# Kernel tuning notes

Measured on AMD Instinct MI355X. Metric: run time of the kernel, lower is better.

## Reference

```python
import jax, jax.numpy as jnp
import numpy as np

HEADS = 16
HEAD_DIM = 128
ROPE_BASE = 10000.0

def _rope_tables(T, D):
    # inv_freq over even indices, freqs = outer(pos, inv_freq), emb = concat([freqs, freqs])
    inv_freq = 1.0 / (ROPE_BASE ** (jnp.arange(0, D, 2, dtype=jnp.float32) / D))
    t = jnp.arange(T, dtype=jnp.float32)
    freqs = t[:, None] * inv_freq[None, :]          # (T, D/2)
    emb = jnp.concatenate([freqs, freqs], axis=-1)  # (T, D)
    return jnp.cos(emb), jnp.sin(emb)

def _rotate_half(x):
    half = x.shape[-1] // 2
    x1, x2 = x[..., :half], x[..., half:]
    return jnp.concatenate([-x2, x1], axis=-1)

def setup_inputs() -> dict:
    key = jax.random.key(0)
    k1, k2, k3 = jax.random.split(key, 3)
    B, T, dim = 2, 2048, 2048
    inner = HEADS * HEAD_DIM
    x = jax.random.normal(k1, (B, T, dim), dtype=jnp.float32)
    W_qkv = jax.random.normal(k2, (3 * inner, dim), dtype=jnp.float32) * 0.02
    W_proj = jax.random.normal(k3, (dim, inner), dtype=jnp.float32) * 0.02
    return {"x": x, "W_qkv": W_qkv, "W_proj": W_proj}

def reference(x, W_qkv, W_proj):
    B, T, dim = x.shape
    H, D = HEADS, HEAD_DIM
    # QKV projection (Linear with weight (out, in): y = x @ W^T)
    qkv = jnp.einsum('btd,ed->bte', x, W_qkv)          # (B, T, 3*H*D)
    q, k, v = jnp.split(qkv, 3, axis=-1)
    def to_heads(t):
        return t.reshape(B, T, H, D).transpose(0, 2, 1, 3)  # (B, H, T, D)
    q, k, v = to_heads(q), to_heads(k), to_heads(v)
    # RoPE, offset = 0 (uncached path)
    cos, sin = _rope_tables(T, D)                      # (T, D)
    cos = cos[None, None]
    sin = sin[None, None]
    q = q * cos + _rotate_half(q) * sin
    k = k * cos + _rotate_half(k) * sin
    # causal SDPA
    scale = 1.0 / jnp.sqrt(jnp.float32(D))
    scores = jnp.einsum('bhqd,bhkd->bhqk', q, k) * scale
    causal = jnp.tril(jnp.ones((T, T), dtype=bool))
    scores = jnp.where(causal[None, None], scores, jnp.finfo(scores.dtype).min)
    attn = jax.nn.softmax(scores, axis=-1)
    out = jnp.einsum('bhqk,bhkd->bhqd', attn, v)       # (B, H, T, D)
    out = out.transpose(0, 2, 1, 3).reshape(B, T, H * D)
    return jnp.einsum('bti,oi->bto', out, W_proj)      # (B, T, dim)
```

## Files before the change

kernel.cpp:

```cpp
#include <hip/hip_runtime.h>
#include <hip/hip_bf16.h>
#include <stdint.h>

typedef __attribute__((ext_vector_type(8))) short short8;
typedef __attribute__((ext_vector_type(4))) float f32x4;

#define HEADS 16
#define HDIM  128
#define BB    2
#define TT    2048
#define DMODEL 2048
#define INNER 2048
#define E3    6144
#define NTOK  (BB*TT)

__device__ inline void store1(__hip_bfloat16* p, float v) { *p = __float2bfloat16(v); }
__device__ inline void store1(float* p, float v)          { *p = v; }

__device__ inline short bfbits(float v) {
  __hip_bfloat16 h = __float2bfloat16(v);
  return *(short*)&h;
}

__device__ inline void gl_lds16(const __hip_bfloat16* g, __hip_bfloat16* l) {
  __builtin_amdgcn_global_load_lds(
      (const __attribute__((address_space(1))) void*)g,
      (__attribute__((address_space(3))) void*)l, 16, 0, 0);
}

__global__ __launch_bounds__(256)
void cvt_bf16(const float* __restrict__ in, __hip_bfloat16* __restrict__ out, int n)
{
  int i = (blockIdx.x * 256 + threadIdx.x) * 8;
  if (i >= n) return;
  float4 a = *(const float4*)(in + i);
  float4 b = *(const float4*)(in + i + 4);
  short8 r;
  r[0]=bfbits(a.x); r[1]=bfbits(a.y); r[2]=bfbits(a.z); r[3]=bfbits(a.w);
  r[4]=bfbits(b.x); r[5]=bfbits(b.y); r[6]=bfbits(b.z); r[7]=bfbits(b.w);
  *(short8*)(out + i) = r;
}

template<typename TC>
__global__ __launch_bounds__(256, 2)
void gemm_lds(const __hip_bfloat16* __restrict__ A,
              const __hip_bfloat16* __restrict__ B,
              TC* __restrict__ C,
              int M, int N, int K)
{
  __shared__ __hip_bfloat16 sA[128*32];
  __shared__ __hip_bfloat16 sB[128*32];
  const int tid  = threadIdx.x;
  const int lane = tid & 63;
  const int wv   = tid >> 6;
  const int lm   = lane & 15;
  const int quad = lane >> 4;
  const int wm   = (wv >> 1) * 64;
  const int wn   = (wv & 1) * 64;
  const int bm   = blockIdx.y * 128;
  const int bn   = blockIdx.x * 128;

  f32x4 acc[4][4];
  #pragma unroll
  for (int i=0;i<4;i++)
    #pragma unroll
    for (int j=0;j<4;j++) acc[i][j] = (f32x4){0.f,0.f,0.f,0.f};

  const int srow = wv*32 + (lane >> 2);
  const int scol = (lane & 3) * 8;
  const __hip_bfloat16* gA0 = A + (size_t)(bm + srow)*K + scol;
  const __hip_bfloat16* gA1 = gA0 + (size_t)16*K;
  const __hip_bfloat16* gB0 = B + (size_t)(bn + srow)*K + scol;
  const __hip_bfloat16* gB1 = gB0 + (size_t)16*K;
  __hip_bfloat16* lA0 = sA + wv*1024;
  __hip_bfloat16* lA1 = lA0 + 512;
  __hip_bfloat16* lB0 = sB + wv*1024;
  __hip_bfloat16* lB1 = lB0 + 512;

  for (int k0 = 0; k0 < K; k0 += 32) {
    __syncthreads();
    gl_lds16(gA0, lA0);
    gl_lds16(gA1, lA1);
    gl_lds16(gB0, lB0);
    gl_lds16(gB1, lB1);
    gA0 += 32; gA1 += 32; gB0 += 32; gB1 += 32;
    __syncthreads();
    short8 af[4], bf[4];
    #pragma unroll
    for (int t=0;t<4;t++)
      af[t] = *(const short8*)(sA + (wm + t*16 + lm)*32 + quad*8);
    #pragma unroll
    for (int t=0;t<4;t++)
      bf[t] = *(const short8*)(sB + (wn + t*16 + lm)*32 + quad*8);
    #pragma unroll
    for (int i=0;i<4;i++)
      #pragma unroll
      for (int j=0;j<4;j++)
        acc[i][j] = __builtin_amdgcn_mfma_f32_16x16x32_bf16(af[i], bf[j], acc[i][j], 0,0,0);
  }

  const int row0 = bm + wm + quad*4;
  const int col0 = bn + wn + lm;
  #pragma unroll
  for (int i=0;i<4;i++)
    #pragma unroll
    for (int j=0;j<4;j++)
      #pragma unroll
      for (int r=0;r<4;r++)
        store1(C + (size_t)(row0 + i*16 + r)*N + col0 + j*16, acc[i][j][r]);
}

__global__ __launch_bounds__(256, 2)
void gemm_qkv(const __hip_bfloat16* __restrict__ A,
              const __hip_bfloat16* __restrict__ B,
              __hip_bfloat16* __restrict__ Qh,
              __hip_bfloat16* __restrict__ Kh,
              __hip_bfloat16* __restrict__ Vt)
{
  __shared__ __hip_bfloat16 sA[128*32];
  __shared__ __hip_bfloat16 sB[128*32];
  __shared__ __hip_bfloat16 sT[128*130];
  const int tid  = threadIdx.x;
  const int lane = tid & 63;
  const int wv   = tid >> 6;
  const int lm   = lane & 15;
  const int quad = lane >> 4;
  const int wm   = (wv >> 1) * 64;
  const int wn   = (wv & 1) * 64;
  const int bm   = blockIdx.y * 128;
  const int bn   = blockIdx.x * 128;

  f32x4 acc[4][4];
  #pragma unroll
  for (int i=0;i<4;i++)
    #pragma unroll
    for (int j=0;j<4;j++) acc[i][j] = (f32x4){0.f,0.f,0.f,0.f};

  const int srow = wv*32 + (lane >> 2);
  const int scol = (lane & 3) * 8;
  const __hip_bfloat16* gA0 = A + (size_t)(bm + srow)*DMODEL + scol;
  const __hip_bfloat16* gA1 = gA0 + (size_t)16*DMODEL;
  const __hip_bfloat16* gB0 = B + (size_t)(bn + srow)*DMODEL + scol;
  const __hip_bfloat16* gB1 = gB0 + (size_t)16*DMODEL;
  __hip_bfloat16* lA0 = sA + wv*1024;
  __hip_bfloat16* lA1 = lA0 + 512;
  __hip_bfloat16* lB0 = sB + wv*1024;
  __hip_bfloat16* lB1 = lB0 + 512;

  for (int k0 = 0; k0 < DMODEL; k0 += 32) {
    __syncthreads();
    gl_lds16(gA0, lA0);
    gl_lds16(gA1, lA1);
    gl_lds16(gB0, lB0);
    gl_lds16(gB1, lB1);
    gA0 += 32; gA1 += 32; gB0 += 32; gB1 += 32;
    __syncthreads();
    short8 af[4], bf[4];
    #pragma unroll
    for (int t=0;t<4;t++)
      af[t] = *(const short8*)(sA + (wm + t*16 + lm)*32 + quad*8);
    #pragma unroll
    for (int t=0;t<4;t++)
      bf[t] = *(const short8*)(sB + (wn + t*16 + lm)*32 + quad*8);
    #pragma unroll
    for (int i=0;i<4;i++)
      #pragma unroll
      for (int j=0;j<4;j++)
        acc[i][j] = __builtin_amdgcn_mfma_f32_16x16x32_bf16(af[i], bf[j], acc[i][j], 0,0,0);
  }

  const int trow = wm + quad*4;
  const int tcol = wn + lm;
  #pragma unroll
  for (int i=0;i<4;i++)
    #pragma unroll
    for (int j=0;j<4;j++)
      #pragma unroll
      for (int r=0;r<4;r++)
        sT[(trow + i*16 + r)*130 + tcol + j*16] = __float2bfloat16(acc[i][j][r]);
  __syncthreads();

  const int type = bn >> 11;
  const int h    = (bn >> 7) & 15;
  const int bgl  = bm >> 11;
  const int tl0  = bm & (TT-1);
  const size_t bh = (size_t)bgl*HEADS + h;
  const float SCQ = 0.08838834764831845f * 1.4426950408889634f;

  if (type < 2) {
    __hip_bfloat16* dst = (type == 0) ? Qh : Kh;
    const float mul = (type == 0) ? SCQ : 1.0f;
    #pragma unroll
    for (int p=0;p<4;p++) {
      const int rowl = p*32 + (tid >> 3);
      const int d2b  = (tid & 7) * 8;
      const int t    = tl0 + rowl;
      short8 o1, o2;
      #pragma unroll
      for (int k=0;k<8;k++) {
        const int d2 = d2b + k;
        float v1 = __bfloat162float(sT[rowl*130 + d2]);
        float v2 = __bfloat162float(sT[rowl*130 + d2 + 64]);
        float inv = powf(10000.f, -(float)d2 * (1.f/64.f));
        float ang = (float)t * inv;
        float c = cosf(ang), s = sinf(ang);
        o1[k] = bfbits((v1*c - v2*s) * mul);
        o2[k] = bfbits((v2*c + v1*s) * mul);
      }
      __hip_bfloat16* o = dst + (bh*TT + t)*HDIM + d2b;
      *(short8*)o        = o1;
      *(short8*)(o + 64) = o2;
    }
  } else {
    #pragma unroll
    for (int it2=0; it2<8; ++it2) {
      const int sidx = it2*256 + tid;
      const int d  = sidx >> 4;
      const int tc = (sidx & 15) * 8;
      short8 o;
      #pragma unroll
      for (int k=0;k<8;k++) o[k] = *(const short*)&sT[(tc+k)*130 + d];
      *(short8*)(Vt + (bh*HDIM + d)*TT + tl0 + tc) = o;
    }
  }
}

__global__ __launch_bounds__(256, 3)
void flash_attn(const __hip_bfloat16* __restrict__ Qh,
                const __hip_bfloat16* __restrict__ Kh,
                const __hip_bfloat16* __restrict__ Vt,
                __hip_bfloat16* __restrict__ Out)
{
  const int tid  = threadIdx.x;
  const int lane = tid & 63;
  const int wv   = tid >> 6;
  const int lm   = lane & 15;
  const int quad = lane >> 4;
  const int jA   = blockIdx.x;
  const int bh   = blockIdx.y;
  const int b    = bh >> 4;
  const int h    = bh & 15;

  __shared__ __hip_bfloat16 sK[64*136];
  __shared__ __hip_bfloat16 sV[128*72];
  __shared__ __hip_bfloat16 sP[4][16*72];

  const float FML2 = 8.0f * 1.4426950408889634f;

  const int rk0 = tid >> 4;
  const int ck  = (tid & 15) * 8;
  const int dv0 = tid >> 3;
  const int cv  = (tid & 7) * 8;
  const __hip_bfloat16* KpBase = Kh + (size_t)bh*TT*HDIM + (size_t)rk0*HDIM + ck;
  const __hip_bfloat16* VpBase = Vt + (size_t)bh*HDIM*TT + (size_t)dv0*TT + cv;

  #pragma unroll
  for (int pass = 0; pass < 2; ++pass) {
    const int q0 = (pass == 0 ? jA : 31 - jA) * 64;

    short8 aq[4];
    {
      const __hip_bfloat16* qp = Qh + ((size_t)bh*TT + q0 + wv*16 + lm)*HDIM + quad*8;
      #pragma unroll
      for (int kd=0;kd<4;kd++) aq[kd] = *(const short8*)(qp + kd*32);
    }

    float l_p[4] = {0,0,0,0};
    f32x4 acc_o[8];
    #pragma unroll
    for (int i=0;i<8;i++) acc_o[i] = (f32x4){0.f,0.f,0.f,0.f};

    const __hip_bfloat16* Kp = KpBase;
    const __hip_bfloat16* Vp = VpBase;
    short8 pk[4], pv[4];
    #pragma unroll
    for (int it=0;it<4;++it) {
      pk[it] = *(const short8*)(Kp + (size_t)it*16*HDIM);
      pv[it] = *(const short8*)(Vp + (size_t)it*32*TT);
    }
    Kp += (size_t)64*HDIM; Vp += 64;

    for (int kv0 = 0; kv0 <= q0; kv0 += 64) {
      __syncthreads();
      #pragma unroll
      for (int it=0;it<4;++it) {
        *(short8*)(&sK[(it*16 + rk0)*136 + ck]) = pk[it];
        *(short8*)(&sV[(it*32 + dv0)*72 + cv])  = pv[it];
      }
      if (kv0 + 64 <= q0) {
        #pragma unroll
        for (int it=0;it<4;++it) {
          pk[it] = *(const short8*)(Kp + (size_t)it*16*HDIM);
          pv[it] = *(const short8*)(Vp + (size_t)it*32*TT);
        }
        Kp += (size_t)64*HDIM; Vp += 64;
      }
      __syncthreads();

      f32x4 accs[4];
      #pragma unroll
      for (int nt=0;nt<4;nt++) accs[nt] = (f32x4){0.f,0.f,0.f,0.f};
      #pragma unroll
      for (int kd=0;kd<4;kd++)
        #pragma unroll
        for (int nt=0;nt<4;nt++) {
          short8 bk = *(const short8*)(&sK[(nt*16 + lm)*136 + kd*32 + quad*8]);
          accs[nt] = __builtin_amdgcn_mfma_f32_16x16x32_bf16(aq[kd], bk, accs[nt], 0,0,0);
        }

      const int rowb = q0 + wv*16 + quad*4;
      const bool diag = (kv0 == q0);
      #pragma unroll
      for (int nt=0;nt<4;nt++)
        #pragma unroll
        for (int r=0;r<4;r++) {
          float p = exp2f(accs[nt][r] - FML2);
          if (diag && (kv0 + nt*16 + lm > rowb + r)) p = 0.f;
          l_p[r] += p;
          sP[wv][(quad*4 + r)*72 + nt*16 + lm] = __float2bfloat16(p);
        }

      #pragma unroll
      for (int kd2=0;kd2<2;kd2++) {
        short8 ap = *(const short8*)(&sP[wv][lm*72 + kd2*32 + quad*8]);
        #pragma unroll
        for (int nt2=0;nt2<8;nt2++) {
          short8 bvv = *(const short8*)(&sV[(nt2*16 + lm)*72 + kd2*32 + quad*8]);
          acc_o[nt2] = __builtin_amdgcn_mfma_f32_16x16x32_bf16(ap, bvv, acc_o[nt2], 0,0,0);
        }
      }
    }

    #pragma unroll
    for (int off=1; off<16; off<<=1)
      #pragma unroll
      for (int r=0;r<4;r++) l_p[r] += __shfl_xor(l_p[r], off);
    #pragma unroll
    for (int r=0;r<4;r++) l_p[r] = 1.f / l_p[r];

    #pragma unroll
    for (int nt2=0;nt2<8;nt2++)
      #pragma unroll
      for (int r=0;r<4;r++) {
        int t = q0 + wv*16 + quad*4 + r;
        Out[((size_t)b*TT + t)*INNER + (size_t)h*HDIM + nt2*16 + lm] =
          __float2bfloat16(acc_o[nt2][r] * l_p[r]);
      }
  }
}

extern "C" void kernel_launch(void* const* d_in, const int* in_sizes, int n_in,
                              void* d_out, int out_size, void* d_ws, size_t ws_size,
                              hipStream_t stream)
{
  (void)in_sizes; (void)n_in; (void)out_size; (void)ws_size;
  const float* x     = (const float*)d_in[0];
  const float* Wqkv  = (const float*)d_in[1];
  const float* Wproj = (const float*)d_in[2];
  float* out = (float*)d_out;

  char* ws = (char*)d_ws;
  __hip_bfloat16* xb       = (__hip_bfloat16*)ws;
  __hip_bfloat16* attn_out = xb;
  char* p1 = ws + (size_t)NTOK*DMODEL*2;
  __hip_bfloat16* Wqkvb  = (__hip_bfloat16*)p1;
  __hip_bfloat16* Wprojb = (__hip_bfloat16*)p1;
  char* p2 = p1 + (size_t)E3*DMODEL*2;
  const size_t hsz = (size_t)BB*HEADS*TT*HDIM*2;
  __hip_bfloat16* Qh = (__hip_bfloat16*)p2;
  __hip_bfloat16* Kh = (__hip_bfloat16*)(p2 + hsz);
  __hip_bfloat16* Vt = (__hip_bfloat16*)(p2 + 2*hsz);

  const int n_x = NTOK*DMODEL, n_wqkv = E3*DMODEL, n_wproj = DMODEL*INNER;
  cvt_bf16<<<dim3(n_x/(256*8)),    dim3(256), 0, stream>>>(x,    xb,    n_x);
  cvt_bf16<<<dim3(n_wqkv/(256*8)), dim3(256), 0, stream>>>(Wqkv, Wqkvb, n_wqkv);

  gemm_qkv<<<dim3(E3/128, NTOK/128), dim3(256), 0, stream>>>(xb, Wqkvb, Qh, Kh, Vt);

  cvt_bf16<<<dim3(n_wproj/(256*8)), dim3(256), 0, stream>>>(Wproj, Wprojb, n_wproj);

  flash_attn<<<dim3(TT/128, BB*HEADS), dim3(256), 0, stream>>>(Qh, Kh, Vt, attn_out);

  gemm_lds<float>
    <<<dim3(INNER/128, NTOK/128), dim3(256), 0, stream>>>(attn_out, Wprojb, out, NTOK, INNER, DMODEL);
}
```

Measured before the change: 398.2 us.

## Fuse input conversions into one prep kernel with precomputed RoPE table

Merges the x and W_qkv fp32-to-bf16 conversion launches into one prep kernel, which also builds a cos/sin RoPE table. The QKV GEMM epilogue then reads that table instead of calling powf/sinf/cosf per element. The GEMM's shared memory is cut by aliasing the transpose buffer over the A/B tiles, with an added barrier, which may allow higher occupancy. The cost is extra table memory traffic and one more sync in the epilogue.

```diff
diff --git a/kernel.cpp b/kernel.cpp
--- a/kernel.cpp
+++ b/kernel.cpp
@@ -28,17 +28,45 @@
       (__attribute__((address_space(3))) void*)l, 16, 0, 0);
 }
 
-__global__ __launch_bounds__(256)
-void cvt_bf16(const float* __restrict__ in, __hip_bfloat16* __restrict__ out, int n)
-{
-  int i = (blockIdx.x * 256 + threadIdx.x) * 8;
-  if (i >= n) return;
+__device__ inline void cvt8(const float* in, __hip_bfloat16* out, int i) {
   float4 a = *(const float4*)(in + i);
   float4 b = *(const float4*)(in + i + 4);
   short8 r;
   r[0]=bfbits(a.x); r[1]=bfbits(a.y); r[2]=bfbits(a.z); r[3]=bfbits(a.w);
   r[4]=bfbits(b.x); r[5]=bfbits(b.y); r[6]=bfbits(b.z); r[7]=bfbits(b.w);
   *(short8*)(out + i) = r;
+}
+
+#define NBX   (NTOK*DMODEL/2048)
+#define NBW   (E3*DMODEL/2048)
+#define NBT   (TT*64/256)
+__global__ __launch_bounds__(256)
+void prep(const float* __restrict__ x, const float* __restrict__ Wqkv,
+          __hip_bfloat16* __restrict__ xb, __hip_bfloat16* __restrict__ Wqkvb,
+          float2* __restrict__ tab)
+{
+  const int tid = threadIdx.x;
+  int blk = blockIdx.x;
+  if (blk < NBX) {
+    cvt8(x, xb, (blk*256 + tid)*8);
+  } else if (blk < NBX + NBW) {
+    cvt8(Wqkv, Wqkvb, ((blk-NBX)*256 + tid)*8);
+  } else {
+    int idx = (blk - NBX - NBW)*256 + tid;
+    int t  = idx >> 6;
+    int d2 = idx & 63;
+    float inv = powf(10000.f, -(float)d2 * (1.f/64.f));
+    float ang = (float)t * inv;
+    tab[idx] = make_float2(cosf(ang), sinf(ang));
+  }
+}
+
+__global__ __launch_bounds__(256)
+void cvt_bf16(const float* __restrict__ in, __hip_bfloat16* __restrict__ out, int n)
+{
+  int i = (blockIdx.x * 256 + threadIdx.x) * 8;
+  if (i >= n) return;
+  cvt8(in, out, i);
 }
 
 template<typename TC>
@@ -113,13 +141,15 @@
 __global__ __launch_bounds__(256, 2)
 void gemm_qkv(const __hip_bfloat16* __restrict__ A,
               const __hip_bfloat16* __restrict__ B,
+              const float2* __restrict__ tab,
               __hip_bfloat16* __restrict__ Qh,
               __hip_bfloat16* __restrict__ Kh,
               __hip_bfloat16* __restrict__ Vt)
 {
-  __shared__ __hip_bfloat16 sA[128*32];
-  __shared__ __hip_bfloat16 sB[128*32];
-  __shared__ __hip_bfloat16 sT[128*130];
+  __shared__ __hip_bfloat16 smem[128*130];
+  __hip_bfloat16* sA = smem;
+  __hip_bfloat16* sB = smem + 128*32;
+  __hip_bfloat16* sT = smem;
   const int tid  = threadIdx.x;
   const int lane = tid & 63;
   const int wv   = tid >> 6;
@@ -169,6 +199,8 @@
         acc[i][j] = __builtin_amdgcn_mfma_f32_16x16x32_bf16(af[i], bf[j], acc[i][j], 0,0,0);
   }
 
+  __syncthreads();
+
   const int trow = wm + quad*4;
   const int tcol = wn + lm;
   #pragma unroll
@@ -195,17 +227,15 @@
       const int rowl = p*32 + (tid >> 3);
       const int d2b  = (tid & 7) * 8;
       const int t    = tl0 + rowl;
+      const float2* tp = tab + (size_t)t*64 + d2b;
       short8 o1, o2;
       #pragma unroll
       for (int k=0;k<8;k++) {
-        const int d2 = d2b + k;
-        float v1 = __bfloat162float(sT[rowl*130 + d2]);
-        float v2 = __bfloat162float(sT[rowl*130 + d2 + 64]);
-        float inv = powf(10000.f, -(float)d2 * (1.f/64.f));
-        float ang = (float)t * inv;
-        float c = cosf(ang), s = sinf(ang);
-        o1[k] = bfbits((v1*c - v2*s) * mul);
-        o2[k] = bfbits((v2*c + v1*s) * mul);
+        float2 cs = tp[k];
+        float v1 = __bfloat162float(sT[rowl*130 + d2b + k]);
+        float v2 = __bfloat162float(sT[rowl*130 + d2b + k + 64]);
+        o1[k] = bfbits((v1*cs.x - v2*cs.y) * mul);
+        o2[k] = bfbits((v2*cs.x + v1*cs.y) * mul);
       }
       __hip_bfloat16* o = dst + (bh*TT + t)*HDIM + d2b;
       *(short8*)o        = o1;
@@ -366,18 +396,18 @@
   __hip_bfloat16* Wqkvb  = (__hip_bfloat16*)p1;
   __hip_bfloat16* Wprojb = (__hip_bfloat16*)p1;
   char* p2 = p1 + (size_t)E3*DMODEL*2;
+  float2* ropeTab = (float2*)p2;
+  char* p3 = p2 + (size_t)DMODEL*INNER*2;
   const size_t hsz = (size_t)BB*HEADS*TT*HDIM*2;
-  __hip_bfloat16* Qh = (__hip_bfloat16*)p2;
-  __hip_bfloat16* Kh = (__hip_bfloat16*)(p2 + hsz);
-  __hip_bfloat16* Vt = (__hip_bfloat16*)(p2 + 2*hsz);
-
-  const int n_x = NTOK*DMODEL, n_wqkv = E3*DMODEL, n_wproj = DMODEL*INNER;
-  cvt_bf16<<<dim3(n_x/(256*8)),    dim3(256), 0, stream>>>(x,    xb,    n_x);
-  cvt_bf16<<<dim3(n_wqkv/(256*8)), dim3(256), 0, stream>>>(Wqkv, Wqkvb, n_wqkv);
-
-  gemm_qkv<<<dim3(E3/128, NTOK/128), dim3(256), 0, stream>>>(xb, Wqkvb, Qh, Kh, Vt);
-
-  cvt_bf16<<<dim3(n_wproj/(256*8)), dim3(256), 0, stream>>>(Wproj, Wprojb, n_wproj);
+  __hip_bfloat16* Qh = (__hip_bfloat16*)p3;
+  __hip_bfloat16* Kh = (__hip_bfloat16*)(p3 + hsz);
+  __hip_bfloat16* Vt = (__hip_bfloat16*)(p3 + 2*hsz);
+
+  prep<<<dim3(NBX + NBW + NBT), dim3(256), 0, stream>>>(x, Wqkv, xb, Wqkvb, ropeTab);
+
+  gemm_qkv<<<dim3(E3/128, NTOK/128), dim3(256), 0, stream>>>(xb, Wqkvb, ropeTab, Qh, Kh, Vt);
+
+  cvt_bf16<<<dim3(DMODEL*INNER/2048), dim3(256), 0, stream>>>(Wproj, Wprojb, DMODEL*INNER);
 
   flash_attn<<<dim3(TT/128, BB*HEADS), dim3(256), 0, stream>>>(Qh, Kh, Vt, attn_out);
 
```

Result: faster. 384.1 us (-3.5%).
